# Kernel optimization log

Hardware: AMD Instinct MI355X
Metric: run time of the kernel (lower is better)

## Reference

```python
import jax, jax.numpy as jnp
import numpy as np

EPS = 1e-5


def _layernorm(x, w, b):
    mu = jnp.mean(x, axis=-1, keepdims=True)
    xc = x - mu
    var = jnp.mean(xc * xc, axis=-1, keepdims=True)
    return xc * jax.lax.rsqrt(var + EPS) * w + b


def _s5_ssm(u, lam_re, lam_im, log_step, B_re, B_im, C_re, C_im, Dvec):
    # u: [B,L,D]; diagonal complex SSM with ZOH discretization + associative scan
    Lam = lam_re + 1j * lam_im                      # [P]
    step = jnp.exp(log_step)                        # [P]
    Abar = jnp.exp(Lam * step)                      # [P]
    Bbar = ((Abar - 1.0) / Lam)[:, None] * (B_re + 1j * B_im)  # [P,D]
    Bu = jnp.einsum('bld,pd->blp', u.astype(jnp.complex64), Bbar)  # [B,L,P]
    A_el = jnp.broadcast_to(Abar, Bu.shape)

    def binop(e1, e2):
        a1, b1 = e1
        a2, b2 = e2
        return a1 * a2, a2 * b1 + b2

    _, xs = jax.lax.associative_scan(binop, (A_el, Bu), axis=1)  # [B,L,P] complex
    y = jnp.einsum('blp,dp->bld', xs, C_re + 1j * C_im).real + Dvec * u
    return y


def _s5_block(x, an_w, an_b, lam_re, lam_im, log_step, B_re, B_im, C_re, C_im,
              Dvec, fn_w, fn_b, Wenc, Wdec):
    fx = _layernorm(x, an_w, an_b)
    s = _s5_ssm(fx, lam_re, lam_im, log_step, B_re, B_im, C_re, C_im, Dvec)
    z = jax.nn.gelu(s, approximate=False) + fx
    fy = _layernorm(z, fn_w, fn_b)
    h = fy @ Wenc.T                                  # [B,L,2D]
    a, g = jnp.split(h, 2, axis=-1)                  # GEGLU
    return (a * jax.nn.gelu(g, approximate=False)) @ Wdec.T + fy


def setup_inputs() -> dict:
    D = 1048   # d_model
    P = 1048   # state_dim
    NL = 3
    Bsz, L = 4, 4096
    key = jax.random.key(0)
    ks = jax.random.split(key, 20)
    f32 = jnp.float32
    inp = {}
    inp['x'] = jax.random.normal(ks[0], (Bsz, L, 1), f32)
    inp['enc_w'] = jax.random.normal(ks[1], (D, 1), f32)
    inp['enc_b'] = jnp.zeros((D,), f32)
    inp['norm_w'] = jnp.ones((NL, D), f32)
    inp['norm_b'] = jnp.zeros((NL, D), f32)
    inp['attn_norm_w'] = jnp.ones((NL, D), f32)
    inp['attn_norm_b'] = jnp.zeros((NL, D), f32)
    inp['ff_norm_w'] = jnp.ones((NL, D), f32)
    inp['ff_norm_b'] = jnp.zeros((NL, D), f32)
    # stable diagonal dynamics: Re(Lambda) < 0
    inp['lam_re'] = -0.5 * jax.random.uniform(ks[2], (NL, P), f32) - 0.05
    inp['lam_im'] = np.float32(np.pi) * jax.random.normal(ks[3], (NL, P), f32)
    lo, hi = np.float32(np.log(1e-3)), np.float32(np.log(1e-1))
    inp['log_step'] = lo + (hi - lo) * jax.random.uniform(ks[4], (NL, P), f32)
    sB = np.float32(1.0 / np.sqrt(D))
    sC = np.float32(1.0 / np.sqrt(P))
    inp['B_re'] = sB * jax.random.normal(ks[5], (NL, P, D), f32)
    inp['B_im'] = sB * jax.random.normal(ks[6], (NL, P, D), f32)
    inp['C_re'] = sC * jax.random.normal(ks[7], (NL, D, P), f32)
    inp['C_im'] = sC * jax.random.normal(ks[8], (NL, D, P), f32)
    inp['Dvec'] = jax.random.normal(ks[9], (NL, D), f32)
    sW = np.float32(1.0 / np.sqrt(D))
    inp['Wenc'] = sW * jax.random.normal(ks[10], (NL, 2 * D, D), f32)
    inp['Wdec'] = sW * jax.random.normal(ks[11], (NL, D, D), f32)
    inp['head_w'] = sW * jax.random.normal(ks[12], (1, D), f32)
    inp['head_b'] = jnp.zeros((1,), f32)
    return inp


def reference(x, enc_w, enc_b, norm_w, norm_b, attn_norm_w, attn_norm_b,
              ff_norm_w, ff_norm_b, lam_re, lam_im, log_step, B_re, B_im,
              C_re, C_im, Dvec, Wenc, Wdec, head_w, head_b):
    h = x @ enc_w.T + enc_b                          # [B,L,D]
    n_layers = norm_w.shape[0]
    for i in range(n_layers):                        # small fixed loop over layers
        z = _layernorm(h, norm_w[i], norm_b[i])      # prenorm
        z = _s5_block(z, attn_norm_w[i], attn_norm_b[i], lam_re[i], lam_im[i],
                      log_step[i], B_re[i], B_im[i], C_re[i], C_im[i],
                      Dvec[i], ff_norm_w[i], ff_norm_b[i], Wenc[i], Wdec[i])
        h = h + z                                    # residual (dropout = identity in eval)
    pooled = jnp.mean(h, axis=1)                     # [B,D]
    y = (pooled @ head_w.T + head_b).squeeze(-1)     # [B]
    return y
```

## Files before the change

### kernel.cpp

```cpp
#include <hip/hip_runtime.h>
#include <hip/hip_bf16.h>
#include <cstddef>

typedef __hip_bfloat16 bf16;

#define D_MODEL 1048
#define P_DIM   1048
#define NLAYER  3
#define BSZ     4
#define LSEQ    4096
#define BL      (BSZ*LSEQ)
#define BLD     ((size_t)BL*D_MODEL)
#define KP      1056
#define NP      1152
#define BLA     ((size_t)BL*KP)
#define NPKP    ((size_t)NP*KP)

#define NC      64
#define CL      (LSEQ/NC)
#define NSCAN   (BSZ*NC*P_DIM)
#define P2      (P_DIM/2)
#define NSCAN2  (BSZ*NC*P2)

typedef __attribute__((ext_vector_type(8))) short short8;
typedef __attribute__((ext_vector_type(4))) float f32x4;

#define TM 128
#define TN 128
#define TK 32
#define TILE_SH (TM*TK)
#define NGEMM   ((BL/TM)*(NP/TN))
#define KSTEPS  (KP/TK)

__device__ __forceinline__ float gelu_f(float x) {
    return 0.5f * x * (1.f + erff(x * 0.70710678118654752f));
}

__device__ __forceinline__ void tile_coords(int id, int& m0, int& n0) {
    int xcd  = id & 7;
    int slot = id >> 3;
    int xg   = slot / 9;
    int j    = slot - xg*9;
    m0 = (xg*8 + xcd) * TM;
    n0 = j * TN;
}

__device__ __forceinline__ void stage_tile(
    const bf16* __restrict__ src, int row0, int k0, short* lds, int tid)
{
#pragma unroll
    for (int c = 0; c < 2; ++c) {
        int chunk = tid + 256*c;
        int r = chunk >> 2;
        int col = ((chunk ^ (r >> 1)) & 3) * 8;
        __builtin_amdgcn_global_load_lds(
            (const __attribute__((address_space(1))) void*)(src + (size_t)(row0 + r)*KP + k0 + col),
            (__attribute__((address_space(3))) void*)(lds + chunk*8), 16, 0, 0);
    }
}

__device__ __forceinline__ void mfma_step1(
    const short* As, const short* Ws, f32x4 (&acc)[4][4],
    int wm, int wn, int row_in, int qs)
{
    short8 a[4], b[4];
#pragma unroll
    for (int i = 0; i < 4; ++i) {
        a[i] = *(const short8*)&As[(wm + i*16 + row_in)*TK + qs];
        b[i] = *(const short8*)&Ws[(wn + i*16 + row_in)*TK + qs];
    }
#pragma unroll
    for (int i = 0; i < 4; ++i)
#pragma unroll
        for (int j = 0; j < 4; ++j)
            acc[i][j] = __builtin_amdgcn_mfma_f32_16x16x32_bf16(a[i], b[j], acc[i][j], 0, 0, 0);
}

__device__ __forceinline__ void mfma_step2(
    const short* As, const short* W0s, const short* W1s,
    f32x4 (&acc0)[4][4], f32x4 (&acc1)[4][4],
    int wm, int wn, int row_in, int qs)
{
    short8 a[4], b0[4], b1[4];
#pragma unroll
    for (int i = 0; i < 4; ++i) {
        a[i]  = *(const short8*)&As [(wm + i*16 + row_in)*TK + qs];
        b0[i] = *(const short8*)&W0s[(wn + i*16 + row_in)*TK + qs];
        b1[i] = *(const short8*)&W1s[(wn + i*16 + row_in)*TK + qs];
    }
#pragma unroll
    for (int i = 0; i < 4; ++i)
#pragma unroll
        for (int j = 0; j < 4; ++j) {
            acc0[i][j] = __builtin_amdgcn_mfma_f32_16x16x32_bf16(a[i], b0[j], acc0[i][j], 0, 0, 0);
            acc1[i][j] = __builtin_amdgcn_mfma_f32_16x16x32_bf16(a[i], b1[j], acc1[i][j], 0, 0, 0);
        }
}

template <int MODE>
__global__ __launch_bounds__(256, 2) void gemm2o_k(
    const bf16* __restrict__ A, const bf16* __restrict__ W0,
    const bf16* __restrict__ W1,
    bf16* __restrict__ O0, bf16* __restrict__ O1, int N)
{
    __shared__ __align__(16) short As[2][TILE_SH];
    __shared__ __align__(16) short W0s[2][TILE_SH];
    __shared__ __align__(16) short W1s[2][TILE_SH];
    const int tid  = threadIdx.x;
    int m0, n0;
    tile_coords(blockIdx.x, m0, n0);
    const int wave = tid >> 6, lane = tid & 63;
    const int wm = (wave >> 1) * 64, wn = (wave & 1) * 64;
    const int row_in = lane & 15;
    const int qs = (((lane >> 4) ^ (lane >> 1)) & 3) * 8;

    f32x4 acc0[4][4] = {};
    f32x4 acc1[4][4] = {};

    stage_tile(A,  m0, 0,  As[0],  tid);
    stage_tile(W0, n0, 0,  W0s[0], tid);
    stage_tile(W1, n0, 0,  W1s[0], tid);
    stage_tile(A,  m0, 32, As[1],  tid);
    stage_tile(W0, n0, 32, W0s[1], tid);
    stage_tile(W1, n0, 32, W1s[1], tid);

    for (int s = 0; s < KSTEPS - 1; ++s) {
        asm volatile("s_waitcnt vmcnt(6)" ::: "memory");
        __builtin_amdgcn_s_barrier();
        mfma_step2(As[s & 1], W0s[s & 1], W1s[s & 1], acc0, acc1, wm, wn, row_in, qs);
        __builtin_amdgcn_s_barrier();
        if (s < KSTEPS - 2) {
            const int k0 = (s + 2) * TK;
            stage_tile(A,  m0, k0, As[s & 1],  tid);
            stage_tile(W0, n0, k0, W0s[s & 1], tid);
            stage_tile(W1, n0, k0, W1s[s & 1], tid);
        }
    }
    asm volatile("s_waitcnt vmcnt(0)" ::: "memory");
    __builtin_amdgcn_s_barrier();
    mfma_step2(As[(KSTEPS-1) & 1], W0s[(KSTEPS-1) & 1], W1s[(KSTEPS-1) & 1],
               acc0, acc1, wm, wn, row_in, qs);

    const int quad = lane >> 4;
#pragma unroll
    for (int i = 0; i < 4; ++i) {
#pragma unroll
        for (int j = 0; j < 4; ++j) {
            int n = n0 + wn + j*16 + row_in;
#pragma unroll
            for (int r = 0; r < 4; ++r) {
                int m = m0 + wm + i*16 + quad*4 + r;
                size_t o = (size_t)m*KP + n;
                if (MODE == 0) {
                    if (n < N)        { O0[o] = __float2bfloat16(acc0[i][j][r]);
                                        O1[o] = __float2bfloat16(acc1[i][j][r]); }
                    else if (n < KP)  { O0[o] = __float2bfloat16(0.f);
                                        O1[o] = __float2bfloat16(0.f); }
                } else {
                    if (n < N)        O0[o] = __float2bfloat16(acc0[i][j][r] * gelu_f(acc1[i][j][r]));
                    else if (n < KP)  O0[o] = __float2bfloat16(0.f);
                }
            }
        }
    }
}

__global__ __launch_bounds__(256, 2) void gemmC_k(
    const bf16* __restrict__ A0, const bf16* __restrict__ W0,
    const bf16* __restrict__ A1, const bf16* __restrict__ W1,
    const bf16* __restrict__ fx, const float* __restrict__ dv,
    bf16* __restrict__ O, int N)
{
    __shared__ __align__(16) short As[2][TILE_SH];
    __shared__ __align__(16) short Ws[2][TILE_SH];
    const int tid  = threadIdx.x;
    int m0, n0;
    tile_coords(blockIdx.x, m0, n0);
    const int wave = tid >> 6, lane = tid & 63;
    const int wm = (wave >> 1) * 64, wn = (wave & 1) * 64;
    const int row_in = lane & 15;
    const int qs = (((lane >> 4) ^ (lane >> 1)) & 3) * 8;

    f32x4 acc[4][4] = {};

    const int NST = 2*KSTEPS;
    stage_tile(A0, m0, 0,  As[0], tid);
    stage_tile(W0, n0, 0,  Ws[0], tid);
    stage_tile(A0, m0, 32, As[1], tid);
    stage_tile(W0, n0, 32, Ws[1], tid);

    for (int s = 0; s < NST - 1; ++s) {
        asm volatile("s_waitcnt vmcnt(4)" ::: "memory");
        __builtin_amdgcn_s_barrier();
        mfma_step1(As[s & 1], Ws[s & 1], acc, wm, wn, row_in, qs);
        __builtin_amdgcn_s_barrier();
        if (s < NST - 2) {
            int t = s + 2;
            const bf16* A = (t >= KSTEPS) ? A1 : A0;
            const bf16* W = (t >= KSTEPS) ? W1 : W0;
            int kk = (t >= KSTEPS) ? t - KSTEPS : t;
            stage_tile(A, m0, kk*TK, As[s & 1], tid);
            stage_tile(W, n0, kk*TK, Ws[s & 1], tid);
        }
    }
    asm volatile("s_waitcnt vmcnt(0)" ::: "memory");
    __builtin_amdgcn_s_barrier();
    mfma_step1(As[(NST-1) & 1], Ws[(NST-1) & 1], acc, wm, wn, row_in, qs);

    const int quad = lane >> 4;
#pragma unroll
    for (int i = 0; i < 4; ++i) {
#pragma unroll
        for (int j = 0; j < 4; ++j) {
            int n = n0 + wn + j*16 + row_in;
#pragma unroll
            for (int r = 0; r < 4; ++r) {
                int m = m0 + wm + i*16 + quad*4 + r;
                size_t o = (size_t)m*KP + n;
                if (n < N) {
                    float f = __bfloat162float(fx[o]);
                    float t = acc[i][j][r] + dv[n]*f;
                    O[o] = __float2bfloat16(gelu_f(t) + f);
                } else if (n < KP) {
                    O[o] = __float2bfloat16(0.f);
                }
            }
        }
    }
}

__global__ __launch_bounds__(256, 2) void gemmD_k(
    const bf16* __restrict__ A, const bf16* __restrict__ W,
    const bf16* __restrict__ fy, float* __restrict__ h, int N)
{
    __shared__ __align__(16) short As[2][TILE_SH];
    __shared__ __align__(16) short Ws[2][TILE_SH];
    const int tid  = threadIdx.x;
    int m0, n0;
    tile_coords(blockIdx.x, m0, n0);
    const int wave = tid >> 6, lane = tid & 63;
    const int wm = (wave >> 1) * 64, wn = (wave & 1) * 64;
    const int row_in = lane & 15;
    const int qs = (((lane >> 4) ^ (lane >> 1)) & 3) * 8;

    f32x4 acc[4][4] = {};

    stage_tile(A, m0, 0,  As[0], tid);
    stage_tile(W, n0, 0,  Ws[0], tid);
    stage_tile(A, m0, 32, As[1], tid);
    stage_tile(W, n0, 32, Ws[1], tid);

    for (int s = 0; s < KSTEPS - 1; ++s) {
        asm volatile("s_waitcnt vmcnt(4)" ::: "memory");
        __builtin_amdgcn_s_barrier();
        mfma_step1(As[s & 1], Ws[s & 1], acc, wm, wn, row_in, qs);
        __builtin_amdgcn_s_barrier();
        if (s < KSTEPS - 2) {
            const int k0 = (s + 2) * TK;
            stage_tile(A, m0, k0, As[s & 1], tid);
            stage_tile(W, n0, k0, Ws[s & 1], tid);
        }
    }
    asm volatile("s_waitcnt vmcnt(0)" ::: "memory");
    __builtin_amdgcn_s_barrier();
    mfma_step1(As[(KSTEPS-1) & 1], Ws[(KSTEPS-1) & 1], acc, wm, wn, row_in, qs);

    const int quad = lane >> 4;
#pragma unroll
    for (int i = 0; i < 4; ++i) {
#pragma unroll
        for (int j = 0; j < 4; ++j) {
            int n = n0 + wn + j*16 + row_in;
            if (n >= N) continue;
#pragma unroll
            for (int r = 0; r < 4; ++r) {
                int m = m0 + wm + i*16 + quad*4 + r;
                float f = __bfloat162float(fy[(size_t)m*KP + n]);
                h[(size_t)m*D_MODEL + n] += acc[i][j][r] + f;
            }
        }
    }
}

__global__ __launch_bounds__(256) void convw5_k(
    const float* __restrict__ s0, const float* __restrict__ s1,
    const float* __restrict__ s2, const float* __restrict__ s3,
    const float* __restrict__ s4, bf16* __restrict__ dst)
{
    size_t i = (size_t)blockIdx.x*256 + threadIdx.x;
    if (i >= NPKP) return;
    int z = blockIdx.z;
    const float* src = (z == 0) ? s0 : (z == 1) ? s1 : (z == 2) ? s2 : (z == 3) ? s3 : s4;
    float scale = (z == 1) ? -1.f : 1.f;
    int n = (int)(i / KP), k = (int)(i - (size_t)n*KP);
    float v = (n < D_MODEL && k < D_MODEL) ? scale*src[(size_t)n*D_MODEL + k] : 0.f;
    dst[(size_t)z*NPKP + i] = __float2bfloat16(v);
}

__device__ __forceinline__ float2 block_reduce2(float a, float b) {
    __syncthreads();
    for (int off = 32; off; off >>= 1) {
        a += __shfl_down(a, off, 64);
        b += __shfl_down(b, off, 64);
    }
    __shared__ float sa[4], sb[4];
    int lane = threadIdx.x & 63, wv = threadIdx.x >> 6;
    if (lane == 0) { sa[wv] = a; sb[wv] = b; }
    __syncthreads();
    if (threadIdx.x == 0) {
        sa[0] = sa[0]+sa[1]+sa[2]+sa[3];
        sb[0] = sb[0]+sb[1]+sb[2]+sb[3];
    }
    __syncthreads();
    return make_float2(sa[0], sb[0]);
}

template <int ENC>
__global__ __launch_bounds__(256) void ln2x_k(
    const float* __restrict__ xin,
    const float* __restrict__ ew, const float* __restrict__ eb,
    float* __restrict__ hbuf,
    const float* __restrict__ w1, const float* __restrict__ bb1,
    const float* __restrict__ w2, const float* __restrict__ bb2,
    bf16* __restrict__ y)
{
    const size_t row = blockIdx.x;
    float v[5];
    float s = 0.f, ss = 0.f;
    int i = 0;
    if (ENC) {
        float xv = xin[row];
        float* hr = hbuf + row * D_MODEL;
        for (int d = threadIdx.x; d < KP; d += 256, ++i) {
            float t = 0.f;
            if (d < D_MODEL) { t = xv*ew[d] + eb[d]; hr[d] = t; }
            v[i] = t; s += t; ss += t*t;
        }
    } else {
        const float* xr = hbuf + row * D_MODEL;
        for (int d = threadIdx.x; d < KP; d += 256, ++i) {
            float t = (d < D_MODEL) ? xr[d] : 0.f;
            v[i] = t; s += t; ss += t*t;
        }
    }
    float2 r = block_reduce2(s, ss);
    float mu  = r.x * (1.f/D_MODEL);
    float var = r.y * (1.f/D_MODEL) - mu*mu;
    float inv = rsqrtf(var + 1e-5f);
    s = 0.f; ss = 0.f; i = 0;
    for (int d = threadIdx.x; d < KP; d += 256, ++i) {
        float z = (d < D_MODEL) ? (v[i]-mu)*inv*w1[d] + bb1[d] : 0.f;
        v[i] = z; s += z; ss += z*z;
    }
    r = block_reduce2(s, ss);
    mu  = r.x * (1.f/D_MODEL);
    var = r.y * (1.f/D_MODEL) - mu*mu;
    inv = rsqrtf(var + 1e-5f);
    bf16* yr = y + row * KP;
    i = 0;
    for (int d = threadIdx.x; d < KP; d += 256, ++i) {
        float o = (d < D_MODEL) ? (v[i]-mu)*inv*w2[d] + bb2[d] : 0.f;
        yr[d] = __float2bfloat16(o);
    }
}

__global__ __launch_bounds__(256) void ln_k(
    const bf16* __restrict__ x, const float* __restrict__ w,
    const float* __restrict__ b, bf16* __restrict__ y)
{
    const size_t row = blockIdx.x;
    const bf16* xr = x + row * KP;
    float v[5];
    float s = 0.f, ss = 0.f;
    int i = 0;
    for (int d = threadIdx.x; d < KP; d += 256, ++i) {
        float t = (d < D_MODEL) ? __bfloat162float(xr[d]) : 0.f;
        v[i] = t; s += t; ss += t*t;
    }
    float2 r = block_reduce2(s, ss);
    float mu  = r.x * (1.f/D_MODEL);
    float var = r.y * (1.f/D_MODEL) - mu*mu;
    float inv = rsqrtf(var + 1e-5f);
    bf16* yr = y + row * KP;
    i = 0;
    for (int d = threadIdx.x; d < KP; d += 256, ++i) {
        float o = (d < D_MODEL) ? (v[i]-mu)*inv*w[d] + b[d] : 0.f;
        yr[d] = __float2bfloat16(o);
    }
}

__global__ __launch_bounds__(256) void prep_k(
    const float* __restrict__ lam_re, const float* __restrict__ lam_im,
    const float* __restrict__ log_step,
    const float* __restrict__ B_re, const float* __restrict__ B_im,
    bf16* __restrict__ bbar_re, bf16* __restrict__ bbar_im,
    float* __restrict__ abar)
{
    size_t idx = (size_t)blockIdx.x*256 + threadIdx.x;
    if (idx >= NPKP) return;
    int p = (int)(idx / KP);
    int d = (int)(idx - (size_t)p*KP);
    if (p >= P_DIM || d >= D_MODEL) {
        bbar_re[idx] = __float2bfloat16(0.f);
        bbar_im[idx] = __float2bfloat16(0.f);
        return;
    }
    float lr = lam_re[p], li = lam_im[p];
    float st = expf(log_step[p]);
    float er = expf(lr*st);
    float ar = er * cosf(li*st);
    float ai = er * sinf(li*st);
    if (d == 0) { abar[p] = ar; abar[P_DIM + p] = ai; }
    float den = lr*lr + li*li;
    float xr = ar - 1.f, xi = ai;
    float cr = (xr*lr + xi*li) / den;
    float ci = (xi*lr - xr*li) / den;
    float br = B_re[(size_t)p*D_MODEL + d], bi = B_im[(size_t)p*D_MODEL + d];
    bbar_re[idx] = __float2bfloat16(cr*br - ci*bi);
// ... 47 lines not shown
    const float* __restrict__ sum_re, const float* __restrict__ sum_im,
    const float* __restrict__ abar,
    float* __restrict__ car_re, float* __restrict__ car_im)
{
    int idx = blockIdx.x*256 + threadIdx.x;
    if (idx >= BSZ*P_DIM) return;
    int p = idx % P_DIM, b = idx / P_DIM;
    float cr = abar[p], ci = abar[P_DIM + p];
#pragma unroll
    for (int s = 0; s < 6; ++s) {
        float nr = cr*cr - ci*ci;
        float ni = 2.f*cr*ci;
        cr = nr; ci = ni;
    }
    float xre = 0.f, xim = 0.f;
    size_t base = (size_t)b*NC*P_DIM + p;
    for (int c = 0; c < NC; ++c) {
        size_t o = base + (size_t)c*P_DIM;
        car_re[o] = xre; car_im[o] = xim;
        float sre = sum_re[o], sim = sum_im[o];
        float nr = fmaf(cr, xre, fmaf(-ci, xim, sre));
        float ni = fmaf(cr, xim, fmaf( ci, xre, sim));
        xre = nr; xim = ni;
    }
}

__global__ __launch_bounds__(256) void scan_apply_k(
    unsigned int* __restrict__ ur, unsigned int* __restrict__ ui,
    const float* __restrict__ abar,
    const float* __restrict__ car_re, const float* __restrict__ car_im)
{
    int idx = blockIdx.x*256 + threadIdx.x;
    if (idx >= NSCAN2) return;
    int p2 = idx % P2;
    int rest = idx / P2;
    int c = rest % NC, b = rest / NC;
    int p = 2*p2;
    float ar0 = abar[p],   ai0 = abar[P_DIM + p];
    float ar1 = abar[p+1], ai1 = abar[P_DIM + p + 1];
    size_t co = ((size_t)b*NC + c)*P_DIM + p;
    float2 c_r = *(const float2*)&car_re[co];
    float2 c_i = *(const float2*)&car_im[co];
    float x0r = c_r.x, x0i = c_i.x, x1r = c_r.y, x1i = c_i.y;
    size_t base = (((size_t)b*LSEQ + (size_t)c*CL)*KP + p) >> 1;
    for (int i = 0; i < CL; ++i) {
        size_t o = base + (size_t)i*(KP/2);
        float2 br = bf2f(ur[o]);
        float2 bi = bf2f(ui[o]);
        float n0r = fmaf(ar0, x0r, fmaf(-ai0, x0i, br.x));
        float n0i = fmaf(ar0, x0i, fmaf( ai0, x0r, bi.x));
        float n1r = fmaf(ar1, x1r, fmaf(-ai1, x1i, br.y));
        float n1i = fmaf(ar1, x1i, fmaf( ai1, x1r, bi.y));
        x0r = n0r; x0i = n0i; x1r = n1r; x1i = n1i;
        ur[o] = f2bf2(x0r, x1r);
        ui[o] = f2bf2(x0i, x1i);
    }
}

__global__ void head_init_k(float* out, const float* hb)
{
    if (threadIdx.x < BSZ) out[threadIdx.x] = hb[0];
}

__global__ __launch_bounds__(256) void head_k(
    const float* __restrict__ h, const float* __restrict__ hw,
    float* __restrict__ out)
{
    int b = blockIdx.x;
    int chunk = blockIdx.y;
    const float* hb = h + ((size_t)b*LSEQ + (size_t)chunk*64)*D_MODEL;
    float s = 0.f;
    for (int l = 0; l < 64; ++l) {
        const float* hr = hb + (size_t)l*D_MODEL;
        for (int d = threadIdx.x; d < D_MODEL; d += 256)
            s += hr[d]*hw[d];
    }
    for (int off = 32; off; off >>= 1) s += __shfl_down(s, off, 64);
    __shared__ float sm[4];
    int lane = threadIdx.x & 63, wv = threadIdx.x >> 6;
    if (lane == 0) sm[wv] = s;
    __syncthreads();
    if (threadIdx.x == 0)
        atomicAdd(out + b, (sm[0]+sm[1]+sm[2]+sm[3]) * (1.f/LSEQ));
}

extern "C" void kernel_launch(void* const* d_in, const int* in_sizes, int n_in,
                              void* d_out, int out_size, void* d_ws, size_t ws_size,
                              hipStream_t stream)
{
    const float* x          = (const float*)d_in[0];
    const float* enc_w      = (const float*)d_in[1];
    const float* enc_b      = (const float*)d_in[2];
    const float* norm_w     = (const float*)d_in[3];
    const float* norm_b     = (const float*)d_in[4];
    const float* attn_w     = (const float*)d_in[5];
    const float* attn_b     = (const float*)d_in[6];
    const float* ff_w       = (const float*)d_in[7];
    const float* ff_b       = (const float*)d_in[8];
    const float* lam_re     = (const float*)d_in[9];
    const float* lam_im     = (const float*)d_in[10];
    const float* log_step   = (const float*)d_in[11];
    const float* B_re       = (const float*)d_in[12];
    const float* B_im       = (const float*)d_in[13];
    const float* C_re       = (const float*)d_in[14];
    const float* C_im       = (const float*)d_in[15];
    const float* Dvec       = (const float*)d_in[16];
    const float* Wenc       = (const float*)d_in[17];
    const float* Wdec       = (const float*)d_in[18];
    const float* head_w     = (const float*)d_in[19];
    const float* head_b     = (const float*)d_in[20];
    float* out = (float*)d_out;

    float* h    = (float*)d_ws;
    bf16*  b1   = (bf16*)(h + BLD);
    bf16*  b2   = b1 + BLA;
    bf16*  b3   = b2 + BLA;
    bf16*  b4   = b3 + BLA;
    bf16*  wbr  = b4 + BLA;
    bf16*  wbi  = wbr + NPKP;
    bf16*  w5   = wbi + NPKP;
    bf16*  wcr  = w5;
    bf16*  wci  = w5 + NPKP;
    bf16*  wea  = w5 + 2*NPKP;
    bf16*  weg  = w5 + 3*NPKP;
    bf16*  wd   = w5 + 4*NPKP;
    float* abar = (float*)(w5 + 5*NPKP);
    float* sum_re = abar + 2*P_DIM;
    float* sum_im = sum_re + NSCAN;
    float* car_re = sum_im + NSCAN;
    float* car_im = car_re + NSCAN;

    const int CV   = (int)((NPKP + 255)/256);
    const int SC_G = (NSCAN2 + 255)/256;
    const size_t pd = (size_t)P_DIM*D_MODEL;

    for (int i = 0; i < NLAYER; ++i) {
        prep_k<<<CV, 256, 0, stream>>>(
            lam_re + i*P_DIM, lam_im + i*P_DIM, log_step + i*P_DIM,
            B_re + i*pd, B_im + i*pd, wbr, wbi, abar);
        const float* WencA = Wenc + (size_t)i*2*pd;
        const float* WencG = WencA + pd;
        convw5_k<<<dim3(CV,1,5), 256, 0, stream>>>(
            C_re + i*pd, C_im + i*pd, WencA, WencG, Wdec + i*pd, w5);

        if (i == 0)
            ln2x_k<1><<<BL, 256, 0, stream>>>(x, enc_w, enc_b, h,
                norm_w + i*D_MODEL, norm_b + i*D_MODEL,
                attn_w + i*D_MODEL, attn_b + i*D_MODEL, b2);
        else
            ln2x_k<0><<<BL, 256, 0, stream>>>(nullptr, nullptr, nullptr, h,
                norm_w + i*D_MODEL, norm_b + i*D_MODEL,
                attn_w + i*D_MODEL, attn_b + i*D_MODEL, b2);

        gemm2o_k<0><<<NGEMM, 256, 0, stream>>>(b2, wbr, wbi, b1, b3, P_DIM);

        scan_partial_k<<<SC_G, 256, 0, stream>>>((unsigned int*)b1, (unsigned int*)b3,
                                                 abar, sum_re, sum_im);
        scan_carry_k<<<(BSZ*P_DIM + 255)/256, 256, 0, stream>>>(sum_re, sum_im, abar, car_re, car_im);
        scan_apply_k<<<SC_G, 256, 0, stream>>>((unsigned int*)b1, (unsigned int*)b3,
                                               abar, car_re, car_im);

        gemmC_k<<<NGEMM, 256, 0, stream>>>(b1, wcr, b3, wci, b2, Dvec + i*D_MODEL, b4, D_MODEL);

        ln_k<<<BL, 256, 0, stream>>>(b4, ff_w + i*D_MODEL, ff_b + i*D_MODEL, b1);

        gemm2o_k<1><<<NGEMM, 256, 0, stream>>>(b1, wea, weg, b2, nullptr, D_MODEL);

        gemmD_k<<<NGEMM, 256, 0, stream>>>(b2, wd, b1, h, D_MODEL);
    }

    head_init_k<<<1, 64, 0, stream>>>(out, head_b);
    head_k<<<dim3(BSZ, 64), 256, 0, stream>>>(h, head_w, out);
}
```

Before: 2.020 ms.

## Split dual-output GEMM across 8 waves and exchange GEGLU gate via LDS

The dual-weight GEMM now runs 512-thread blocks where half the waves compute against W0 and half against W1, so each wave holds one accumulator set instead of two. This roughly halves per-thread register pressure and allows higher occupancy. In GEGLU mode the gate accumulators are passed through shared memory so the other waves can apply the product, at the cost of extra barriers and LDS traffic in the epilogue. The launch bounds of the other GEMMs are also raised to allow 3 blocks per CU, which may force register spills.

```diff
diff --git a/kernel.cpp b/kernel.cpp
--- a/kernel.cpp
+++ b/kernel.cpp
@@ -59,6 +59,16 @@
     }
 }
 
+__device__ __forceinline__ void stage512(
+    const bf16* __restrict__ src, int row0, int k0, short* lds, int tid)
+{
+    int r = tid >> 2;
+    int col = ((tid ^ (r >> 1)) & 3) * 8;
+    __builtin_amdgcn_global_load_lds(
+        (const __attribute__((address_space(1))) void*)(src + (size_t)(row0 + r)*KP + k0 + col),
+        (__attribute__((address_space(3))) void*)(lds + tid*8), 16, 0, 0);
+}
+
 __device__ __forceinline__ void mfma_step1(
     const short* As, const short* Ws, f32x4 (&acc)[4][4],
     int wm, int wn, int row_in, int qs)
@@ -76,96 +86,112 @@
             acc[i][j] = __builtin_amdgcn_mfma_f32_16x16x32_bf16(a[i], b[j], acc[i][j], 0, 0, 0);
 }
 
-__device__ __forceinline__ void mfma_step2(
-    const short* As, const short* W0s, const short* W1s,
-    f32x4 (&acc0)[4][4], f32x4 (&acc1)[4][4],
-    int wm, int wn, int row_in, int qs)
-{
-    short8 a[4], b0[4], b1[4];
-#pragma unroll
-    for (int i = 0; i < 4; ++i) {
-        a[i]  = *(const short8*)&As [(wm + i*16 + row_in)*TK + qs];
-        b0[i] = *(const short8*)&W0s[(wn + i*16 + row_in)*TK + qs];
-        b1[i] = *(const short8*)&W1s[(wn + i*16 + row_in)*TK + qs];
-    }
-#pragma unroll
-    for (int i = 0; i < 4; ++i)
-#pragma unroll
-        for (int j = 0; j < 4; ++j) {
-            acc0[i][j] = __builtin_amdgcn_mfma_f32_16x16x32_bf16(a[i], b0[j], acc0[i][j], 0, 0, 0);
-            acc1[i][j] = __builtin_amdgcn_mfma_f32_16x16x32_bf16(a[i], b1[j], acc1[i][j], 0, 0, 0);
-        }
-}
-
 template <int MODE>
-__global__ __launch_bounds__(256, 2) void gemm2o_k(
+__global__ __launch_bounds__(512, 4) void gemm2o_k(
     const bf16* __restrict__ A, const bf16* __restrict__ W0,
     const bf16* __restrict__ W1,
     bf16* __restrict__ O0, bf16* __restrict__ O1, int N)
 {
-    __shared__ __align__(16) short As[2][TILE_SH];
-    __shared__ __align__(16) short W0s[2][TILE_SH];
-    __shared__ __align__(16) short W1s[2][TILE_SH];
+    __shared__ __align__(16) short smem[6*TILE_SH];
+    short* As  = smem;
+    short* W0s = smem + 2*TILE_SH;
+    short* W1s = smem + 4*TILE_SH;
     const int tid  = threadIdx.x;
     int m0, n0;
     tile_coords(blockIdx.x, m0, n0);
     const int wave = tid >> 6, lane = tid & 63;
-    const int wm = (wave >> 1) * 64, wn = (wave & 1) * 64;
+    const int wr = wave >> 2, wc = wave & 3;
+    const int wm = wr * 64;
+    const int wn = (wc & 1) * 64;
+    const bool useW1 = (wc >= 2);
     const int row_in = lane & 15;
     const int qs = (((lane >> 4) ^ (lane >> 1)) & 3) * 8;
 
-    f32x4 acc0[4][4] = {};
-    f32x4 acc1[4][4] = {};
-
-    stage_tile(A,  m0, 0,  As[0],  tid);
-    stage_tile(W0, n0, 0,  W0s[0], tid);
-    stage_tile(W1, n0, 0,  W1s[0], tid);
-    stage_tile(A,  m0, 32, As[1],  tid);
-    stage_tile(W0, n0, 32, W0s[1], tid);
-    stage_tile(W1, n0, 32, W1s[1], tid);
+    f32x4 acc[4][4] = {};
+
+    stage512(A,  m0, 0,  As,             tid);
+    stage512(W0, n0, 0,  W0s,            tid);
+    stage512(W1, n0, 0,  W1s,            tid);
+    stage512(A,  m0, 32, As  + TILE_SH,  tid);
+    stage512(W0, n0, 32, W0s + TILE_SH,  tid);
+    stage512(W1, n0, 32, W1s + TILE_SH,  tid);
 
     for (int s = 0; s < KSTEPS - 1; ++s) {
-        asm volatile("s_waitcnt vmcnt(6)" ::: "memory");
+        asm volatile("s_waitcnt vmcnt(3)" ::: "memory");
         __builtin_amdgcn_s_barrier();
-        mfma_step2(As[s & 1], W0s[s & 1], W1s[s & 1], acc0, acc1, wm, wn, row_in, qs);
+        const int off = (s & 1) * TILE_SH;
+        const short* Ws = (useW1 ? W1s : W0s) + off;
+        mfma_step1(As + off, Ws, acc, wm, wn, row_in, qs);
         __builtin_amdgcn_s_barrier();
         if (s < KSTEPS - 2) {
             const int k0 = (s + 2) * TK;
-            stage_tile(A,  m0, k0, As[s & 1],  tid);
-            stage_tile(W0, n0, k0, W0s[s & 1], tid);
-            stage_tile(W1, n0, k0, W1s[s & 1], tid);
+            stage512(A,  m0, k0, As  + off, tid);
+            stage512(W0, n0, k0, W0s + off, tid);
+            stage512(W1, n0, k0, W1s + off, tid);
         }
     }
     asm volatile("s_waitcnt vmcnt(0)" ::: "memory");
     __builtin_amdgcn_s_barrier();
-    mfma_step2(As[(KSTEPS-1) & 1], W0s[(KSTEPS-1) & 1], W1s[(KSTEPS-1) & 1],
-               acc0, acc1, wm, wn, row_in, qs);
+    {
+        const int off = ((KSTEPS-1) & 1) * TILE_SH;
+        const short* Ws = (useW1 ? W1s : W0s) + off;
+        mfma_step1(As + off, Ws, acc, wm, wn, row_in, qs);
+    }
 
     const int quad = lane >> 4;
-#pragma unroll
-    for (int i = 0; i < 4; ++i) {
-#pragma unroll
-        for (int j = 0; j < 4; ++j) {
-            int n = n0 + wn + j*16 + row_in;
-#pragma unroll
-            for (int r = 0; r < 4; ++r) {
-                int m = m0 + wm + i*16 + quad*4 + r;
-                size_t o = (size_t)m*KP + n;
-                if (MODE == 0) {
-                    if (n < N)        { O0[o] = __float2bfloat16(acc0[i][j][r]);
-                                        O1[o] = __float2bfloat16(acc1[i][j][r]); }
-                    else if (n < KP)  { O0[o] = __float2bfloat16(0.f);
-                                        O1[o] = __float2bfloat16(0.f); }
-                } else {
-                    if (n < N)        O0[o] = __float2bfloat16(acc0[i][j][r] * gelu_f(acc1[i][j][r]));
-                    else if (n < KP)  O0[o] = __float2bfloat16(0.f);
+    if (MODE == 0) {
+        bf16* O = useW1 ? O1 : O0;
+#pragma unroll
+        for (int i = 0; i < 4; ++i) {
+#pragma unroll
+            for (int j = 0; j < 4; ++j) {
+                int n = n0 + wn + j*16 + row_in;
+#pragma unroll
+                for (int r = 0; r < 4; ++r) {
+                    int m = m0 + wm + i*16 + quad*4 + r;
+                    size_t o = (size_t)m*KP + n;
+                    if (n < N)        O[o] = __float2bfloat16(acc[i][j][r]);
+                    else if (n < KP)  O[o] = __float2bfloat16(0.f);
                 }
             }
         }
-    }
-}
-
-__global__ __launch_bounds__(256, 2) void gemmC_k(
+    } else {
+        f32x4* xb = (f32x4*)smem;
+        const int pp = wr*2 + (wc & 1);
+#pragma unroll
+        for (int ih = 0; ih < 2; ++ih) {
+            __syncthreads();
+            if (useW1) {
+#pragma unroll
+                for (int il = 0; il < 2; ++il)
+#pragma unroll
+                    for (int j = 0; j < 4; ++j)
+                        xb[(((pp*2 + il)*4 + j) << 6) + lane] = acc[2*ih + il][j];
+            }
+            __syncthreads();
+            if (!useW1) {
+#pragma unroll
+                for (int il = 0; il < 2; ++il) {
+                    int i = 2*ih + il;
+#pragma unroll
+                    for (int j = 0; j < 4; ++j) {
+                        f32x4 g = xb[(((pp*2 + il)*4 + j) << 6) + lane];
+                        int n = n0 + wn + j*16 + row_in;
+#pragma unroll
+                        for (int r = 0; r < 4; ++r) {
+                            int m = m0 + wm + i*16 + quad*4 + r;
+                            size_t o = (size_t)m*KP + n;
+                            if (n < N)        O0[o] = __float2bfloat16(acc[i][j][r] * gelu_f(g[r]));
+                            else if (n < KP)  O0[o] = __float2bfloat16(0.f);
+                        }
+                    }
+                }
+            }
+        }
+    }
+}
+
+__global__ __launch_bounds__(256, 3) void gemmC_k(
     const bf16* __restrict__ A0, const bf16* __restrict__ W0,
     const bf16* __restrict__ A1, const bf16* __restrict__ W1,
     const bf16* __restrict__ fx, const float* __restrict__ dv,
@@ -229,7 +255,7 @@
     }
 }
 
-__global__ __launch_bounds__(256, 2) void gemmD_k(
+__global__ __launch_bounds__(256, 3) void gemmD_k(
     const bf16* __restrict__ A, const bf16* __restrict__ W,
     const bf16* __restrict__ fy, float* __restrict__ h, int N)
 {
@@ -617,7 +643,7 @@
                 norm_w + i*D_MODEL, norm_b + i*D_MODEL,
                 attn_w + i*D_MODEL, attn_b + i*D_MODEL, b2);
 
-        gemm2o_k<0><<<NGEMM, 256, 0, stream>>>(b2, wbr, wbi, b1, b3, P_DIM);
+        gemm2o_k<0><<<NGEMM, 512, 0, stream>>>(b2, wbr, wbi, b1, b3, P_DIM);
 
         scan_partial_k<<<SC_G, 256, 0, stream>>>((unsigned int*)b1, (unsigned int*)b3,
                                                  abar, sum_re, sum_im);
@@ -629,7 +655,7 @@
 
         ln_k<<<BL, 256, 0, stream>>>(b4, ff_w + i*D_MODEL, ff_b + i*D_MODEL, b1);
 
-        gemm2o_k<1><<<NGEMM, 256, 0, stream>>>(b1, wea, weg, b2, nullptr, D_MODEL);
+        gemm2o_k<1><<<NGEMM, 512, 0, stream>>>(b1, wea, weg, b2, nullptr, D_MODEL);
 
         gemmD_k<<<NGEMM, 256, 0, stream>>>(b2, wd, b1, h, D_MODEL);
     }
```

Result: slower. 2.080 ms (+3.0%).

## Split dual-output GEMMs into single-output kernels with higher occupancy and setprio

Applied to the files above, without the earlier changes.

Replaces the dual-weight GEMM kernels, which held two accumulator sets and three LDS tiles, with a single-output GEMM template. The B-projection now launches two grid slices for the real and imaginary weights. The GEGLU GEMM becomes two launches: one writes gelu(g) to a buffer and the second multiplies by it in its epilogue. Launch bounds rise to 3 blocks per SM and s_setprio wraps the MFMA sections. The aim is lower register and LDS pressure for better latency hiding, at the cost of reloading the A tiles twice and an extra round trip of the gelu intermediate through memory.

```diff
diff --git a/kernel.cpp b/kernel.cpp
--- a/kernel.cpp
+++ b/kernel.cpp
@@ -76,36 +76,95 @@
             acc[i][j] = __builtin_amdgcn_mfma_f32_16x16x32_bf16(a[i], b[j], acc[i][j], 0, 0, 0);
 }
 
-__device__ __forceinline__ void mfma_step2(
-    const short* As, const short* W0s, const short* W1s,
-    f32x4 (&acc0)[4][4], f32x4 (&acc1)[4][4],
-    int wm, int wn, int row_in, int qs)
-{
-    short8 a[4], b0[4], b1[4];
+template <int NPASS>
+__device__ __forceinline__ void kloop(
+    const bf16* __restrict__ A0, const bf16* __restrict__ W0,
+    const bf16* __restrict__ A1, const bf16* __restrict__ W1,
+    int m0, int n0, short* sA, short* sW,
+    f32x4 (&acc)[4][4], int tid, int wm, int wn, int row_in, int qs)
+{
+    const int NST = NPASS*KSTEPS;
+    stage_tile(A0, m0, 0,  sA,           tid);
+    stage_tile(W0, n0, 0,  sW,           tid);
+    stage_tile(A0, m0, TK, sA + TILE_SH, tid);
+    stage_tile(W0, n0, TK, sW + TILE_SH, tid);
+    for (int s = 0; s < NST - 1; ++s) {
+        asm volatile("s_waitcnt vmcnt(4)" ::: "memory");
+        __builtin_amdgcn_s_barrier();
+        const int off = (s & 1)*TILE_SH;
+        __builtin_amdgcn_s_setprio(1);
+        mfma_step1(sA + off, sW + off, acc, wm, wn, row_in, qs);
+        __builtin_amdgcn_s_setprio(0);
+        __builtin_amdgcn_s_barrier();
+        if (s < NST - 2) {
+            int t = s + 2;
+            const bf16* A = (NPASS == 2 && t >= KSTEPS) ? A1 : A0;
+            const bf16* W = (NPASS == 2 && t >= KSTEPS) ? W1 : W0;
+            int kk = (NPASS == 2 && t >= KSTEPS) ? t - KSTEPS : t;
+            stage_tile(A, m0, kk*TK, sA + off, tid);
+            stage_tile(W, n0, kk*TK, sW + off, tid);
+        }
+    }
+    asm volatile("s_waitcnt vmcnt(0)" ::: "memory");
+    __builtin_amdgcn_s_barrier();
+    const int off = ((NST-1) & 1)*TILE_SH;
+    __builtin_amdgcn_s_setprio(1);
+    mfma_step1(sA + off, sW + off, acc, wm, wn, row_in, qs);
+    __builtin_amdgcn_s_setprio(0);
+}
+
+template <int EPI>
+__global__ __launch_bounds__(256, 3) void gemmS_k(
+    const bf16* __restrict__ A, const bf16* __restrict__ W0,
+    const bf16* __restrict__ W1, const bf16* __restrict__ G,
+    bf16* __restrict__ O0, bf16* __restrict__ O1, int N)
+{
+    __shared__ __align__(16) short sA[2*TILE_SH];
+    __shared__ __align__(16) short sW[2*TILE_SH];
+    const int tid  = threadIdx.x;
+    int m0, n0;
+    tile_coords(blockIdx.x, m0, n0);
+    const bf16* W = blockIdx.y ? W1 : W0;
+    bf16*       O = blockIdx.y ? O1 : O0;
+    const int wave = tid >> 6, lane = tid & 63;
+    const int wm = (wave >> 1) * 64, wn = (wave & 1) * 64;
+    const int row_in = lane & 15;
+    const int qs = (((lane >> 4) ^ (lane >> 1)) & 3) * 8;
+
+    f32x4 acc[4][4] = {};
+    kloop<1>(A, W, nullptr, nullptr, m0, n0, sA, sW, acc, tid, wm, wn, row_in, qs);
+
+    const int quad = lane >> 4;
 #pragma unroll
     for (int i = 0; i < 4; ++i) {
-        a[i]  = *(const short8*)&As [(wm + i*16 + row_in)*TK + qs];
-        b0[i] = *(const short8*)&W0s[(wn + i*16 + row_in)*TK + qs];
-        b1[i] = *(const short8*)&W1s[(wn + i*16 + row_in)*TK + qs];
-    }
-#pragma unroll
-    for (int i = 0; i < 4; ++i)
 #pragma unroll
         for (int j = 0; j < 4; ++j) {
-            acc0[i][j] = __builtin_amdgcn_mfma_f32_16x16x32_bf16(a[i], b0[j], acc0[i][j], 0, 0, 0);
-            acc1[i][j] = __builtin_amdgcn_mfma_f32_16x16x32_bf16(a[i], b1[j], acc1[i][j], 0, 0, 0);
+            int n = n0 + wn + j*16 + row_in;
+#pragma unroll
+            for (int r = 0; r < 4; ++r) {
+                int m = m0 + wm + i*16 + quad*4 + r;
+                size_t o = (size_t)m*KP + n;
+                if (n < N) {
+                    float v = acc[i][j][r];
+                    if (EPI == 1) v = gelu_f(v);
+                    if (EPI == 2) v *= __bfloat162float(G[o]);
+                    O[o] = __float2bfloat16(v);
+                } else if (n < KP) {
+                    O[o] = __float2bfloat16(0.f);
+                }
+            }
         }
-}
-
-template <int MODE>
-__global__ __launch_bounds__(256, 2) void gemm2o_k(
-    const bf16* __restrict__ A, const bf16* __restrict__ W0,
-    const bf16* __restrict__ W1,
-    bf16* __restrict__ O0, bf16* __restrict__ O1, int N)
-{
-    __shared__ __align__(16) short As[2][TILE_SH];
-    __shared__ __align__(16) short W0s[2][TILE_SH];
-    __shared__ __align__(16) short W1s[2][TILE_SH];
+    }
+}
+
+__global__ __launch_bounds__(256, 3) void gemmC_k(
+    const bf16* __restrict__ A0, const bf16* __restrict__ W0,
+    const bf16* __restrict__ A1, const bf16* __restrict__ W1,
+    const bf16* __restrict__ fx, const float* __restrict__ dv,
+    bf16* __restrict__ O, int N)
+{
+    __shared__ __align__(16) short sA[2*TILE_SH];
+    __shared__ __align__(16) short sW[2*TILE_SH];
     const int tid  = threadIdx.x;
     int m0, n0;
     tile_coords(blockIdx.x, m0, n0);
@@ -114,98 +173,8 @@
     const int row_in = lane & 15;
     const int qs = (((lane >> 4) ^ (lane >> 1)) & 3) * 8;
 
-    f32x4 acc0[4][4] = {};
-    f32x4 acc1[4][4] = {};
-
-    stage_tile(A,  m0, 0,  As[0],  tid);
-    stage_tile(W0, n0, 0,  W0s[0], tid);
-    stage_tile(W1, n0, 0,  W1s[0], tid);
-    stage_tile(A,  m0, 32, As[1],  tid);
-    stage_tile(W0, n0, 32, W0s[1], tid);
-    stage_tile(W1, n0, 32, W1s[1], tid);
-
-    for (int s = 0; s < KSTEPS - 1; ++s) {
-        asm volatile("s_waitcnt vmcnt(6)" ::: "memory");
-        __builtin_amdgcn_s_barrier();
-        mfma_step2(As[s & 1], W0s[s & 1], W1s[s & 1], acc0, acc1, wm, wn, row_in, qs);
-        __builtin_amdgcn_s_barrier();
-        if (s < KSTEPS - 2) {
-            const int k0 = (s + 2) * TK;
-            stage_tile(A,  m0, k0, As[s & 1],  tid);
-            stage_tile(W0, n0, k0, W0s[s & 1], tid);
-            stage_tile(W1, n0, k0, W1s[s & 1], tid);
-        }
-    }
-    asm volatile("s_waitcnt vmcnt(0)" ::: "memory");
-    __builtin_amdgcn_s_barrier();
-    mfma_step2(As[(KSTEPS-1) & 1], W0s[(KSTEPS-1) & 1], W1s[(KSTEPS-1) & 1],
-               acc0, acc1, wm, wn, row_in, qs);
-
-    const int quad = lane >> 4;
-#pragma unroll
-    for (int i = 0; i < 4; ++i) {
-#pragma unroll
-        for (int j = 0; j < 4; ++j) {
-            int n = n0 + wn + j*16 + row_in;
-#pragma unroll
-            for (int r = 0; r < 4; ++r) {
-                int m = m0 + wm + i*16 + quad*4 + r;
-                size_t o = (size_t)m*KP + n;
-                if (MODE == 0) {
-                    if (n < N)        { O0[o] = __float2bfloat16(acc0[i][j][r]);
-                                        O1[o] = __float2bfloat16(acc1[i][j][r]); }
-                    else if (n < KP)  { O0[o] = __float2bfloat16(0.f);
-                                        O1[o] = __float2bfloat16(0.f); }
-                } else {
-                    if (n < N)        O0[o] = __float2bfloat16(acc0[i][j][r] * gelu_f(acc1[i][j][r]));
-                    else if (n < KP)  O0[o] = __float2bfloat16(0.f);
-                }
-            }
-        }
-    }
-}
-
-__global__ __launch_bounds__(256, 2) void gemmC_k(
-    const bf16* __restrict__ A0, const bf16* __restrict__ W0,
-    const bf16* __restrict__ A1, const bf16* __restrict__ W1,
-    const bf16* __restrict__ fx, const float* __restrict__ dv,
-    bf16* __restrict__ O, int N)
-{
-    __shared__ __align__(16) short As[2][TILE_SH];
-    __shared__ __align__(16) short Ws[2][TILE_SH];
-    const int tid  = threadIdx.x;
-    int m0, n0;
-    tile_coords(blockIdx.x, m0, n0);
-    const int wave = tid >> 6, lane = tid & 63;
-    const int wm = (wave >> 1) * 64, wn = (wave & 1) * 64;
-    const int row_in = lane & 15;
-    const int qs = (((lane >> 4) ^ (lane >> 1)) & 3) * 8;
-
     f32x4 acc[4][4] = {};
-
-    const int NST = 2*KSTEPS;
-    stage_tile(A0, m0, 0,  As[0], tid);
-    stage_tile(W0, n0, 0,  Ws[0], tid);
-    stage_tile(A0, m0, 32, As[1], tid);
-    stage_tile(W0, n0, 32, Ws[1], tid);
-
-    for (int s = 0; s < NST - 1; ++s) {
-        asm volatile("s_waitcnt vmcnt(4)" ::: "memory");
-        __builtin_amdgcn_s_barrier();
-        mfma_step1(As[s & 1], Ws[s & 1], acc, wm, wn, row_in, qs);
-        __builtin_amdgcn_s_barrier();
-        if (s < NST - 2) {
-            int t = s + 2;
-            const bf16* A = (t >= KSTEPS) ? A1 : A0;
-            const bf16* W = (t >= KSTEPS) ? W1 : W0;
-            int kk = (t >= KSTEPS) ? t - KSTEPS : t;
-            stage_tile(A, m0, kk*TK, As[s & 1], tid);
-            stage_tile(W, n0, kk*TK, Ws[s & 1], tid);
-        }
-    }
-    asm volatile("s_waitcnt vmcnt(0)" ::: "memory");
-    __builtin_amdgcn_s_barrier();
-    mfma_step1(As[(NST-1) & 1], Ws[(NST-1) & 1], acc, wm, wn, row_in, qs);
+    kloop<2>(A0, W0, A1, W1, m0, n0, sA, sW, acc, tid, wm, wn, row_in, qs);
 
     const int quad = lane >> 4;
 #pragma unroll
@@ -229,12 +198,12 @@
     }
 }
 
-__global__ __launch_bounds__(256, 2) void gemmD_k(
+__global__ __launch_bounds__(256, 3) void gemmD_k(
     const bf16* __restrict__ A, const bf16* __restrict__ W,
     const bf16* __restrict__ fy, float* __restrict__ h, int N)
 {
-    __shared__ __align__(16) short As[2][TILE_SH];
-    __shared__ __align__(16) short Ws[2][TILE_SH];
+    __shared__ __align__(16) short sA[2*TILE_SH];
+    __shared__ __align__(16) short sW[2*TILE_SH];
     const int tid  = threadIdx.x;
     int m0, n0;
     tile_coords(blockIdx.x, m0, n0);
@@ -244,26 +213,7 @@
     const int qs = (((lane >> 4) ^ (lane >> 1)) & 3) * 8;
 
     f32x4 acc[4][4] = {};
-
-    stage_tile(A, m0, 0,  As[0], tid);
-    stage_tile(W, n0, 0,  Ws[0], tid);
-    stage_tile(A, m0, 32, As[1], tid);
-    stage_tile(W, n0, 32, Ws[1], tid);
-
-    for (int s = 0; s < KSTEPS - 1; ++s) {
-        asm volatile("s_waitcnt vmcnt(4)" ::: "memory");
-        __builtin_amdgcn_s_barrier();
-        mfma_step1(As[s & 1], Ws[s & 1], acc, wm, wn, row_in, qs);
-        __builtin_amdgcn_s_barrier();
-        if (s < KSTEPS - 2) {
-            const int k0 = (s + 2) * TK;
-            stage_tile(A, m0, k0, As[s & 1], tid);
-            stage_tile(W, n0, k0, Ws[s & 1], tid);
-        }
-    }
-    asm volatile("s_waitcnt vmcnt(0)" ::: "memory");
-    __builtin_amdgcn_s_barrier();
-    mfma_step1(As[(KSTEPS-1) & 1], Ws[(KSTEPS-1) & 1], acc, wm, wn, row_in, qs);
+    kloop<1>(A, W, nullptr, nullptr, m0, n0, sA, sW, acc, tid, wm, wn, row_in, qs);
 
     const int quad = lane >> 4;
 #pragma unroll
@@ -617,7 +567,8 @@
                 norm_w + i*D_MODEL, norm_b + i*D_MODEL,
                 attn_w + i*D_MODEL, attn_b + i*D_MODEL, b2);
 
-        gemm2o_k<0><<<NGEMM, 256, 0, stream>>>(b2, wbr, wbi, b1, b3, P_DIM);
+        gemmS_k<0><<<dim3(NGEMM, 2), 256, 0, stream>>>(
+            b2, wbr, wbi, nullptr, b1, b3, P_DIM);
 
         scan_partial_k<<<SC_G, 256, 0, stream>>>((unsigned int*)b1, (unsigned int*)b3,
                                                  abar, sum_re, sum_im);
@@ -629,7 +580,10 @@
 
         ln_k<<<BL, 256, 0, stream>>>(b4, ff_w + i*D_MODEL, ff_b + i*D_MODEL, b1);
 
-        gemm2o_k<1><<<NGEMM, 256, 0, stream>>>(b1, wea, weg, b2, nullptr, D_MODEL);
+        gemmS_k<1><<<dim3(NGEMM, 1), 256, 0, stream>>>(
+            b1, weg, nullptr, nullptr, b4, nullptr, D_MODEL);
+        gemmS_k<2><<<dim3(NGEMM, 1), 256, 0, stream>>>(
+            b1, wea, nullptr, b4, b2, nullptr, D_MODEL);
 
         gemmD_k<<<NGEMM, 256, 0, stream>>>(b2, wd, b1, h, D_MODEL);
     }
```

Measured after the change: 2.137 ms. 1.06x slower.

## Use 256x128 GEMM tiles with 512 threads and a four-stage LDS pipeline

Applied to the files above, without the earlier changes.

All four GEMM kernels move from 128x128 tiles with 256 threads and double buffering to 256x128 tiles with 512 threads and a four-slot ring buffer. Each step now needs one barrier instead of two, prefetches three stages ahead, and raises wave priority around the MFMA block. The goal is to hide more global-load latency and reuse each loaded W tile across more rows. The larger LDS footprint (about 128 KB for gemm2) and higher register pressure may limit how many blocks fit on a CU, and there are half as many blocks.

```diff
diff --git a/kernel.cpp b/kernel.cpp
--- a/kernel.cpp
+++ b/kernel.cpp
@@ -25,12 +25,15 @@
 typedef __attribute__((ext_vector_type(8))) short short8;
 typedef __attribute__((ext_vector_type(4))) float f32x4;
 
-#define TM 128
-#define TN 128
+#define BM 256
+#define BN 128
 #define TK 32
-#define TILE_SH (TM*TK)
-#define NGEMM   ((BL/TM)*(NP/TN))
+#define ASH (BM*TK)
+#define BSH (BN*TK)
+#define SLOT1 (ASH + BSH)
+#define SLOT2 (ASH + 2*BSH)
 #define KSTEPS  (KP/TK)
+#define NG2   ((BL/BM)*(NP/BN))
 
 __device__ __forceinline__ float gelu_f(float x) {
     return 0.5f * x * (1.f + erff(x * 0.70710678118654752f));
@@ -41,22 +44,31 @@
     int slot = id >> 3;
     int xg   = slot / 9;
     int j    = slot - xg*9;
-    m0 = (xg*8 + xcd) * TM;
-    n0 = j * TN;
-}
-
-__device__ __forceinline__ void stage_tile(
+    m0 = (xg*8 + xcd) * BM;
+    n0 = j * BN;
+}
+
+__device__ __forceinline__ void stageA256(
     const bf16* __restrict__ src, int row0, int k0, short* lds, int tid)
 {
 #pragma unroll
-    for (int c = 0; c < 2; ++c) {
-        int chunk = tid + 256*c;
-        int r = chunk >> 2;
-        int col = ((chunk ^ (r >> 1)) & 3) * 8;
+    for (int c0 = 0; c0 < 2; ++c0) {
+        int c = tid + 512*c0;
+        int r = c >> 2;
+        int col = ((c ^ (r >> 1)) & 3) * 8;
         __builtin_amdgcn_global_load_lds(
             (const __attribute__((address_space(1))) void*)(src + (size_t)(row0 + r)*KP + k0 + col),
-            (__attribute__((address_space(3))) void*)(lds + chunk*8), 16, 0, 0);
-    }
+            (__attribute__((address_space(3))) void*)(lds + c*8), 16, 0, 0);
+    }
+}
+__device__ __forceinline__ void stageB128(
+    const bf16* __restrict__ src, int row0, int k0, short* lds, int tid)
+{
+    int r = tid >> 2;
+    int col = ((tid ^ (r >> 1)) & 3) * 8;
+    __builtin_amdgcn_global_load_lds(
+        (const __attribute__((address_space(1))) void*)(src + (size_t)(row0 + r)*KP + k0 + col),
+        (__attribute__((address_space(3))) void*)(lds + tid*8), 16, 0, 0);
 }
 
 __device__ __forceinline__ void mfma_step1(
@@ -97,15 +109,43 @@
         }
 }
 
+template <int NPASS>
+__device__ __forceinline__ void kloop1(
+    const bf16* __restrict__ A0, const bf16* __restrict__ W0,
+    const bf16* __restrict__ A1, const bf16* __restrict__ W1,
+    int m0, int n0, short* sm,
+    f32x4 (&acc)[4][4], int tid, int wm, int wn, int row_in, int qs)
+{
+    const int NST = NPASS*KSTEPS;
+#define STAGE1(t) { int _t = (t); \
+        const bf16* _A = (NPASS == 2 && _t >= KSTEPS) ? A1 : A0; \
+        const bf16* _W = (NPASS == 2 && _t >= KSTEPS) ? W1 : W0; \
+        int _kk = (NPASS == 2 && _t >= KSTEPS) ? _t - KSTEPS : _t; \
+        short* _b = sm + (_t & 3)*SLOT1; \
+        stageA256(_A, m0, _kk*TK, _b, tid); \
+        stageB128(_W, n0, _kk*TK, _b + ASH, tid); }
+    STAGE1(0); STAGE1(1); STAGE1(2);
+    for (int s = 0; s < NST; ++s) {
+        if (s < NST - 2)       asm volatile("s_waitcnt vmcnt(6)" ::: "memory");
+        else if (s == NST - 2) asm volatile("s_waitcnt vmcnt(3)" ::: "memory");
+        else                   asm volatile("s_waitcnt vmcnt(0)" ::: "memory");
+        __builtin_amdgcn_s_barrier();
+        if (s < NST - 3) STAGE1(s + 3);
+        short* base = sm + (s & 3)*SLOT1;
+        __builtin_amdgcn_s_setprio(1);
+        mfma_step1(base, base + ASH, acc, wm, wn, row_in, qs);
+        __builtin_amdgcn_s_setprio(0);
+    }
+#undef STAGE1
+}
+
 template <int MODE>
-__global__ __launch_bounds__(256, 2) void gemm2o_k(
+__global__ __launch_bounds__(512, 2) void gemm2_k(
     const bf16* __restrict__ A, const bf16* __restrict__ W0,
     const bf16* __restrict__ W1,
     bf16* __restrict__ O0, bf16* __restrict__ O1, int N)
 {
-    __shared__ __align__(16) short As[2][TILE_SH];
-    __shared__ __align__(16) short W0s[2][TILE_SH];
-    __shared__ __align__(16) short W1s[2][TILE_SH];
+    __shared__ __align__(16) short sm[4*SLOT2];
     const int tid  = threadIdx.x;
     int m0, n0;
     tile_coords(blockIdx.x, m0, n0);
@@ -117,29 +157,24 @@
     f32x4 acc0[4][4] = {};
     f32x4 acc1[4][4] = {};
 
-    stage_tile(A,  m0, 0,  As[0],  tid);
-    stage_tile(W0, n0, 0,  W0s[0], tid);
-    stage_tile(W1, n0, 0,  W1s[0], tid);
-    stage_tile(A,  m0, 32, As[1],  tid);
-    stage_tile(W0, n0, 32, W0s[1], tid);
-    stage_tile(W1, n0, 32, W1s[1], tid);
-
-    for (int s = 0; s < KSTEPS - 1; ++s) {
-        asm volatile("s_waitcnt vmcnt(6)" ::: "memory");
+#define STAGE2(t) { int _t = (t); \
+        short* _b = sm + (_t & 3)*SLOT2; \
+        stageA256(A,  m0, _t*TK, _b, tid); \
+        stageB128(W0, n0, _t*TK, _b + ASH, tid); \
+        stageB128(W1, n0, _t*TK, _b + ASH + BSH, tid); }
+    STAGE2(0); STAGE2(1); STAGE2(2);
+    for (int s = 0; s < KSTEPS; ++s) {
+        if (s < KSTEPS - 2)       asm volatile("s_waitcnt vmcnt(8)" ::: "memory");
+        else if (s == KSTEPS - 2) asm volatile("s_waitcnt vmcnt(4)" ::: "memory");
+        else                      asm volatile("s_waitcnt vmcnt(0)" ::: "memory");
         __builtin_amdgcn_s_barrier();
-        mfma_step2(As[s & 1], W0s[s & 1], W1s[s & 1], acc0, acc1, wm, wn, row_in, qs);
-        __builtin_amdgcn_s_barrier();
-        if (s < KSTEPS - 2) {
-            const int k0 = (s + 2) * TK;
-            stage_tile(A,  m0, k0, As[s & 1],  tid);
-            stage_tile(W0, n0, k0, W0s[s & 1], tid);
-            stage_tile(W1, n0, k0, W1s[s & 1], tid);
-        }
-    }
-    asm volatile("s_waitcnt vmcnt(0)" ::: "memory");
-    __builtin_amdgcn_s_barrier();
-    mfma_step2(As[(KSTEPS-1) & 1], W0s[(KSTEPS-1) & 1], W1s[(KSTEPS-1) & 1],
-               acc0, acc1, wm, wn, row_in, qs);
+        if (s < KSTEPS - 3) STAGE2(s + 3);
+        short* base = sm + (s & 3)*SLOT2;
+        __builtin_amdgcn_s_setprio(1);
+        mfma_step2(base, base + ASH, base + ASH + BSH, acc0, acc1, wm, wn, row_in, qs);
+        __builtin_amdgcn_s_setprio(0);
+    }
+#undef STAGE2
 
     const int quad = lane >> 4;
 #pragma unroll
@@ -165,14 +200,13 @@
     }
 }
 
-__global__ __launch_bounds__(256, 2) void gemmC_k(
+__global__ __launch_bounds__(512, 2) void gemmC_k(
     const bf16* __restrict__ A0, const bf16* __restrict__ W0,
     const bf16* __restrict__ A1, const bf16* __restrict__ W1,
     const bf16* __restrict__ fx, const float* __restrict__ dv,
     bf16* __restrict__ O, int N)
 {
-    __shared__ __align__(16) short As[2][TILE_SH];
-    __shared__ __align__(16) short Ws[2][TILE_SH];
+    __shared__ __align__(16) short sm[4*SLOT1];
     const int tid  = threadIdx.x;
     int m0, n0;
     tile_coords(blockIdx.x, m0, n0);
@@ -182,30 +216,7 @@
     const int qs = (((lane >> 4) ^ (lane >> 1)) & 3) * 8;
 
     f32x4 acc[4][4] = {};
-
-    const int NST = 2*KSTEPS;
-    stage_tile(A0, m0, 0,  As[0], tid);
-    stage_tile(W0, n0, 0,  Ws[0], tid);
-    stage_tile(A0, m0, 32, As[1], tid);
-    stage_tile(W0, n0, 32, Ws[1], tid);
-
-    for (int s = 0; s < NST - 1; ++s) {
-        asm volatile("s_waitcnt vmcnt(4)" ::: "memory");
-        __builtin_amdgcn_s_barrier();
-        mfma_step1(As[s & 1], Ws[s & 1], acc, wm, wn, row_in, qs);
-        __builtin_amdgcn_s_barrier();
-        if (s < NST - 2) {
-            int t = s + 2;
-            const bf16* A = (t >= KSTEPS) ? A1 : A0;
-            const bf16* W = (t >= KSTEPS) ? W1 : W0;
-            int kk = (t >= KSTEPS) ? t - KSTEPS : t;
-            stage_tile(A, m0, kk*TK, As[s & 1], tid);
-            stage_tile(W, n0, kk*TK, Ws[s & 1], tid);
-        }
-    }
-    asm volatile("s_waitcnt vmcnt(0)" ::: "memory");
-    __builtin_amdgcn_s_barrier();
-    mfma_step1(As[(NST-1) & 1], Ws[(NST-1) & 1], acc, wm, wn, row_in, qs);
+    kloop1<2>(A0, W0, A1, W1, m0, n0, sm, acc, tid, wm, wn, row_in, qs);
 
     const int quad = lane >> 4;
 #pragma unroll
@@ -229,12 +240,11 @@
     }
 }
 
-__global__ __launch_bounds__(256, 2) void gemmD_k(
+__global__ __launch_bounds__(512, 2) void gemmD_k(
     const bf16* __restrict__ A, const bf16* __restrict__ W,
     const bf16* __restrict__ fy, float* __restrict__ h, int N)
 {
-    __shared__ __align__(16) short As[2][TILE_SH];
-    __shared__ __align__(16) short Ws[2][TILE_SH];
+    __shared__ __align__(16) short sm[4*SLOT1];
     const int tid  = threadIdx.x;
     int m0, n0;
     tile_coords(blockIdx.x, m0, n0);
@@ -244,26 +254,7 @@
     const int qs = (((lane >> 4) ^ (lane >> 1)) & 3) * 8;
 
     f32x4 acc[4][4] = {};
-
-    stage_tile(A, m0, 0,  As[0], tid);
-    stage_tile(W, n0, 0,  Ws[0], tid);
-    stage_tile(A, m0, 32, As[1], tid);
-    stage_tile(W, n0, 32, Ws[1], tid);
-
-    for (int s = 0; s < KSTEPS - 1; ++s) {
-        asm volatile("s_waitcnt vmcnt(4)" ::: "memory");
-        __builtin_amdgcn_s_barrier();
-        mfma_step1(As[s & 1], Ws[s & 1], acc, wm, wn, row_in, qs);
-        __builtin_amdgcn_s_barrier();
-        if (s < KSTEPS - 2) {
-            const int k0 = (s + 2) * TK;
-            stage_tile(A, m0, k0, As[s & 1], tid);
-            stage_tile(W, n0, k0, Ws[s & 1], tid);
-        }
-    }
-    asm volatile("s_waitcnt vmcnt(0)" ::: "memory");
-    __builtin_amdgcn_s_barrier();
-    mfma_step1(As[(KSTEPS-1) & 1], Ws[(KSTEPS-1) & 1], acc, wm, wn, row_in, qs);
+    kloop1<1>(A, W, nullptr, nullptr, m0, n0, sm, acc, tid, wm, wn, row_in, qs);
 
     const int quad = lane >> 4;
 #pragma unroll
@@ -617,7 +608,7 @@
                 norm_w + i*D_MODEL, norm_b + i*D_MODEL,
                 attn_w + i*D_MODEL, attn_b + i*D_MODEL, b2);
 
-        gemm2o_k<0><<<NGEMM, 256, 0, stream>>>(b2, wbr, wbi, b1, b3, P_DIM);
+        gemm2_k<0><<<NG2, 512, 0, stream>>>(b2, wbr, wbi, b1, b3, P_DIM);
 
         scan_partial_k<<<SC_G, 256, 0, stream>>>((unsigned int*)b1, (unsigned int*)b3,
                                                  abar, sum_re, sum_im);
@@ -625,13 +616,13 @@
         scan_apply_k<<<SC_G, 256, 0, stream>>>((unsigned int*)b1, (unsigned int*)b3,
                                                abar, car_re, car_im);
 
-        gemmC_k<<<NGEMM, 256, 0, stream>>>(b1, wcr, b3, wci, b2, Dvec + i*D_MODEL, b4, D_MODEL);
+        gemmC_k<<<NG2, 512, 0, stream>>>(b1, wcr, b3, wci, b2, Dvec + i*D_MODEL, b4, D_MODEL);
 
         ln_k<<<BL, 256, 0, stream>>>(b4, ff_w + i*D_MODEL, ff_b + i*D_MODEL, b1);
 
-        gemm2o_k<1><<<NGEMM, 256, 0, stream>>>(b1, wea, weg, b2, nullptr, D_MODEL);
-
-        gemmD_k<<<NGEMM, 256, 0, stream>>>(b2, wd, b1, h, D_MODEL);
+        gemm2_k<1><<<NG2, 512, 0, stream>>>(b1, wea, weg, b2, nullptr, D_MODEL);
+
+        gemmD_k<<<NG2, 512, 0, stream>>>(b2, wd, b1, h, D_MODEL);
     }
 
     head_init_k<<<1, 64, 0, stream>>>(out, head_b);
```

Measured after the change: 2.012 ms. No clear change (-0.4%).
